# Kernel tuning notes

Hardware: AMD Instinct MI355X
Metric: run time of the kernel (lower is better)

The kernel has to match this reference:

```python
import jax, jax.numpy as jnp
import numpy as np

D, E, H, B, T, W = 64, 128, 64, 16, 512, 3
TEMP = 0.05


def setup_inputs() -> dict:
    key = jax.random.key(0)
    ks = jax.random.split(key, 11)
    s = 1.0 / np.sqrt(H)
    return {
        "x1": jax.random.normal(ks[0], (B, T, D), jnp.float32),
        "x2": jax.random.normal(ks[1], (B, T, D), jnp.float32),
        "u": jax.random.uniform(ks[2], (B, T), jnp.float32),
        "wih0": jax.random.normal(ks[3], (2, 4 * H, D), jnp.float32) * s,
        "whh0": jax.random.normal(ks[4], (2, 4 * H, H), jnp.float32) * s,
        "bih0": jax.random.normal(ks[5], (2, 4 * H), jnp.float32) * s,
        "bhh0": jax.random.normal(ks[6], (2, 4 * H), jnp.float32) * s,
        "wih1": jax.random.normal(ks[7], (2, 4 * H, 2 * H), jnp.float32) * s,
        "whh1": jax.random.normal(ks[8], (2, 4 * H, H), jnp.float32) * s,
        "bih1": jax.random.normal(ks[9], (2, 4 * H), jnp.float32) * s,
        "bhh1": jax.random.normal(ks[10], (2, 4 * H), jnp.float32) * s,
    }


def _lstm_dir(x, wi, wh, bi, bh, reverse):
    # x: [B, T, F]; PyTorch gate order i, f, g, o
    xg = jnp.einsum('btf,gf->btg', x, wi) + bi + bh  # [B, T, 4H]

    def step(carry, xg_t):
        h, c = carry
        g = xg_t + h @ wh.T
        i, f, gg, o = jnp.split(g, 4, axis=-1)
        c = jax.nn.sigmoid(f) * c + jax.nn.sigmoid(i) * jnp.tanh(gg)
        h = jax.nn.sigmoid(o) * jnp.tanh(c)
        return (h, c), h

    h0 = jnp.zeros((x.shape[0], H), x.dtype)
    _, hs = jax.lax.scan(step, (h0, h0), jnp.swapaxes(xg, 0, 1), reverse=reverse)
    return jnp.swapaxes(hs, 0, 1)  # [B, T, H]


def _bilstm_layer(x, wih, whh, bih, bhh):
    hf = _lstm_dir(x, wih[0], whh[0], bih[0], bhh[0], False)
    hb = _lstm_dir(x, wih[1], whh[1], bih[1], bhh[1], True)
    return jnp.concatenate([hf, hb], axis=-1)  # [B, T, 2H]


def _embed(x, wih0, whh0, bih0, bhh0, wih1, whh1, bih1, bhh1):
    h = _bilstm_layer(x, wih0, whh0, bih0, bhh0)
    h = _bilstm_layer(h, wih1, whh1, bih1, bhh1)
    # F.normalize(p=2, dim=-1), eps=1e-12
    n = jnp.maximum(jnp.linalg.norm(h, axis=-1, keepdims=True), 1e-12)
    return h / n


def _window_indices(u):
    # vectorized version of the per-step windowed np.random.choice
    # equal lengths: s = (len2 - len1 + 1) / (len1 - 1) = 1 / (T - 1)
    k = jnp.arange(T)
    s = 1.0 / (T - 1)
    center = k + (k * s).astype(jnp.int32)
    lo = jnp.maximum(center - W, 0)
    hi = jnp.minimum(center + W, T)       # slice end is clipped to list length
    count = (hi - lo).astype(jnp.float32)
    i2 = lo[None, :] + jnp.floor(u * count[None, :]).astype(jnp.int32)
    return jnp.minimum(i2, hi[None, :] - 1)  # [B, T]


def reference(x1, x2, u, wih0, whh0, bih0, bhh0, wih1, whh1, bih1, bhh1):
    z1 = _embed(x1, wih0, whh0, bih0, bhh0, wih1, whh1, bih1, bhh1)  # [B,T,E]
    z2 = _embed(x2, wih0, whh0, bih0, bhh0, wih1, whh1, bih1, bhh1)

    i2 = _window_indices(u)                                   # [B, T]
    z2s = jnp.take_along_axis(z2, i2[:, :, None], axis=1)     # [B, T, E]

    a = z1.reshape(-1, E)   # [N, E], N = B*T
    b = z2s.reshape(-1, E)

    # sim_matrix with eps-guarded renormalization (eps=1e-8)
    an = jnp.maximum(jnp.linalg.norm(a, axis=1, keepdims=True), 1e-8)
    bn = jnp.maximum(jnp.linalg.norm(b, axis=1, keepdims=True), 1e-8)
    sim = (a / an) @ (b / bn).T                               # [N, N]
    logits = sim / TEMP

    n = logits.shape[0]
    d = jnp.arange(n)
    lsm_row = jax.nn.log_softmax(logits, axis=1)
    lsm_col = jax.nn.log_softmax(logits, axis=0)
    loss = -(lsm_row[d, d].mean() + lsm_col[d, d].mean())
    return loss
```

## Files before the change

kernel.cpp:

```cpp
#include <hip/hip_runtime.h>
#include <hip/hip_bf16.h>

typedef unsigned short ushort_t;
typedef __attribute__((ext_vector_type(2))) float f32x2;
typedef __attribute__((ext_vector_type(4))) float f32x4;
typedef __attribute__((ext_vector_type(8))) short s16x8;
typedef _Float16 f16;
typedef __attribute__((ext_vector_type(2))) f16 f16x2;
typedef __attribute__((ext_vector_type(8))) f16 f16x8;

#define DEV __device__ __forceinline__

constexpr int MT = 16384;

DEV ushort_t f2bf(float f) {
  union { float f; unsigned u; } un; un.f = f;
  unsigned r = un.u + 0x7FFFu + ((un.u >> 16) & 1u);
  return (ushort_t)(r >> 16);
}
DEV ushort_t f2h(float f) {
  union { f16 h; ushort_t u; } cv; cv.h = (f16)f; return cv.u;
}
DEV float h2f(ushort_t u) {
  union { ushort_t u; f16 h; } cv; cv.u = u; return (float)cv.h;
}
template<int CTRL>
DEV float dppmv(float v) {
  union { float f; int i; } x; x.f = v;
  union { int i; float f; } y;
  y.i = __builtin_amdgcn_mov_dpp(x.i, CTRL, 0xf, 0xf, true);
  return y.f;
}
DEV int TPs(int rev, int t) {
  t = t > 511 ? 511 : t;
  t = t < 0 ? 0 : t;
  return rev ? (511 - t) : t;
}
DEV float sigf(float x) { return __builtin_amdgcn_rcpf(1.f + __expf(-x)); }
DEV float thf(float x)  { return 1.f - 2.f * __builtin_amdgcn_rcpf(1.f + __expf(2.f * x)); }
DEV float fexp2(float x) { float r; asm("v_exp_f32 %0, %1" : "=v"(r) : "v"(x)); return r; }

__global__ void k_idx(const float* __restrict__ u, int* __restrict__ i2) {
  int i = blockIdx.x * 256 + threadIdx.x;
  int t = i & 511;
  float s = 1.0f / 511.0f;
  int center = t + (int)((float)t * s);
  int lo = center - 3; if (lo < 0) lo = 0;
  int hi = center + 3; if (hi > 512) hi = 512;
  float count = (float)(hi - lo);
  int v = lo + (int)floorf(u[i] * count);
  int mx = hi - 1;
  i2[i] = v < mx ? v : mx;
}

__global__ void k_concat(const float* __restrict__ x1, const float* __restrict__ x2,
                         float* __restrict__ out) {
  int i = blockIdx.x * 256 + threadIdx.x;
  const int half = 16 * 512 * 64 / 4;
  float4* o = (float4*)out;
  const float4* a = (const float4*)x1;
  const float4* b = (const float4*)x2;
  o[i] = (i < half) ? a[i] : b[i - half];
}

template<int K>
__global__ __launch_bounds__(256) void k_xgemm(const float* __restrict__ In, const float* __restrict__ Wt,
                                               const float* __restrict__ bih, const float* __restrict__ bhh,
                                               ushort_t* __restrict__ Out) {
  const int bm = blockIdx.x, bn = blockIdx.y, d = blockIdx.z;
  const int tid = threadIdx.x;
  __shared__ float InS[64][128];
  __shared__ float WS[64][65];
  const int tm = tid >> 4, tn = tid & 15;
  float acc[8][4];
#pragma unroll
  for (int r = 0; r < 8; ++r)
#pragma unroll
    for (int c = 0; c < 4; ++c) acc[r][c] = 0.f;

  const int j = tid >> 2;
  const int jg = j >> 4, jt = j & 15;
  const int wn = jg * 64 + bn * 16 + jt;

  for (int kc = 0; kc < K; kc += 64) {
    __syncthreads();
    {
      const int m = tid >> 1;
      const float4* src = (const float4*)(In + (size_t)(bm * 128 + m) * K + kc);
#pragma unroll
      for (int i = 0; i < 8; ++i) {
        const int kq = (tid & 1) * 8 + i;
        float4 v = src[kq];
        InS[kq * 4 + 0][m] = v.x; InS[kq * 4 + 1][m] = v.y;
        InS[kq * 4 + 2][m] = v.z; InS[kq * 4 + 3][m] = v.w;
      }
      const float4* wsrc = (const float4*)(Wt + (size_t)(d * 256 + wn) * K + kc);
#pragma unroll
      for (int i = 0; i < 4; ++i) {
        const int kq = (tid & 3) * 4 + i;
        float4 v = wsrc[kq];
        WS[kq * 4 + 0][j] = v.x; WS[kq * 4 + 1][j] = v.y;
        WS[kq * 4 + 2][j] = v.z; WS[kq * 4 + 3][j] = v.w;
      }
    }
    __syncthreads();
#pragma unroll 8
    for (int k = 0; k < 64; ++k) {
      float4 a0 = *(const float4*)&InS[k][tm * 8];
      float4 a1 = *(const float4*)&InS[k][tm * 8 + 4];
      float av[8] = {a0.x, a0.y, a0.z, a0.w, a1.x, a1.y, a1.z, a1.w};
      float bb[4] = {WS[k][tn], WS[k][16 + tn], WS[k][32 + tn], WS[k][48 + tn]};
#pragma unroll
      for (int r = 0; r < 8; ++r)
#pragma unroll
        for (int c = 0; c < 4; ++c) acc[r][c] += av[r] * bb[c];
    }
  }
  const int u = bn * 16 + tn;
  float bs[4];
#pragma unroll
  for (int g = 0; g < 4; ++g)
    bs[g] = bih[d * 256 + g * 64 + u] + bhh[d * 256 + g * 64 + u];
  const int npb = bn * 64 + tn * 4;
#pragma unroll
  for (int r = 0; r < 8; ++r) {
    ushort4 o;
    o.x = f2h(acc[r][0] + bs[0]);
    o.y = f2h(acc[r][1] + bs[1]);
    o.z = f2h(acc[r][2] + bs[2]);
    o.w = f2h(acc[r][3] + bs[3]);
    *(ushort4*)(Out + ((size_t)d * MT + (size_t)(bm * 128 + tm * 8 + r)) * 256 + npb) = o;
  }
}

constexpr int NCH = 64;
constexpr int CH = 512 / NCH;
constexpr int WARM = 48;
__global__ __launch_bounds__(256) void k_scan10(const ushort_t* __restrict__ xg,
                                                const float* __restrict__ whh,
                                                float* __restrict__ hout) {
  __shared__ ushort_t H[2][1024] __attribute__((aligned(16)));
  const int tid = threadIdx.x;
  const int w = tid >> 6, l = tid & 63;
  const int cl = l & 15, rg = l >> 4;
  const int uq = cl >> 2, g = cl & 3;
  const int d = blockIdx.x >> 1, hf = blockIdx.x & 1;
  const int rev = d;
  const int s_begin = blockIdx.y * CH;
  const int wm = (s_begin < WARM) ? s_begin : WARM;
  const int sstart = s_begin - wm;
  const int nsteps = CH + wm;

  f16x8 Bf[4][2];
#pragma unroll
  for (int nt = 0; nt < 4; ++nt)
#pragma unroll
    for (int kc = 0; kc < 2; ++kc) {
      const int urow = g * 64 + (w * 16 + nt * 4 + uq);
      const float* src = whh + ((size_t)(d * 256 + urow)) * 64 + kc * 32 + rg * 8;
      f16x8 v;
#pragma unroll
      for (int i = 0; i < 8; ++i) v[i] = (f16)src[i];
      Bf[nt][kc] = v;
    }

  ((uint4*)H)[tid] = (uint4){0u, 0u, 0u, 0u};
  float c[4] = {0.f, 0.f, 0.f, 0.f};

  const size_t bbase = ((size_t)(d * 32 + hf * 16)) * 512 * 256;
  float* hcur = hout + ((size_t)(hf * 16) * 512 + (size_t)TPs(rev, sstart)) * 128 + d * 64;
  const int hdir = rev ? -128 : 128;
  int cx[4][4], ho[4];
#pragma unroll
  for (int nt = 0; nt < 4; ++nt) {
#pragma unroll
    for (int j = 0; j < 4; ++j)
      cx[nt][j] = ((rg * 4 + j) * 512) * 256 + w * 64 + nt * 16 + cl;
    ho[nt] = ((rg * 4 + g) * 512) * 128 + w * 16 + nt * 4 + uq;
  }
  const int ab0 = (cl * 128 + rg * 16) ^ ((cl & 7) << 4);
  const int ab1 = (cl * 128 + 64 + rg * 16) ^ ((cl & 7) << 4);
  const int hwoff_m = rg * 4 + g;
  const bool gb0 = (g & 1) != 0, gb1 = (g & 2) != 0;

  float pf0[4][4], pf1[4][4], pf2[4][4], pf3[4][4];
  auto LOADST = [&](int sp, float (&P)[4][4]) {
    const ushort_t* xp = xg + bbase + (size_t)TPs(rev, sstart + sp) * 256;
#pragma unroll
    for (int nt = 0; nt < 4; ++nt)
#pragma unroll
      for (int j = 0; j < 4; ++j) P[nt][j] = h2f(xp[cx[nt][j]]);
  };
  LOADST(0, pf0);
  LOADST(1, pf1);
  LOADST(2, pf2);

  asm volatile("s_waitcnt lgkmcnt(0)" ::: "memory");
  __builtin_amdgcn_s_barrier();
  asm volatile("" ::: "memory");

  auto STEP = [&](int s, float (&PC)[4][4], float (&PN)[4][4]) {
    const char* Hr = (const char*)H[s & 1];
    f16x8 a0 = *(const f16x8*)(Hr + ab0);
    f16x8 a1 = *(const f16x8*)(Hr + ab1);
    f32x4 acc[4];
#pragma unroll
    for (int nt = 0; nt < 4; ++nt) {
      acc[nt] = (f32x4){PC[nt][0], PC[nt][1], PC[nt][2], PC[nt][3]};
      acc[nt] = __builtin_amdgcn_mfma_f32_16x16x32_f16(a0, Bf[nt][0], acc[nt], 0, 0, 0);
      acc[nt] = __builtin_amdgcn_mfma_f32_16x16x32_f16(a1, Bf[nt][1], acc[nt], 0, 0, 0);
    }
    LOADST(s + 3, PN);
    char* Hw = (char*)H[(s & 1) ^ 1];
    float hv[4];
#pragma unroll
    for (int nt = 0; nt < 4; ++nt) {
      float V0 = acc[nt][0], V1 = acc[nt][1], V2 = acc[nt][2], V3 = acc[nt][3];
      float s0 = dppmv<0xB1>(V0);
      float s1 = dppmv<0xB1>(V1);
      float s2 = dppmv<0xB1>(V2);
      float s3 = dppmv<0xB1>(V3);
      asm volatile("" : "+v"(s0), "+v"(s1), "+v"(s2), "+v"(s3));
      float W0 = gb0 ? s1 : V0;
      float W1 = gb0 ? V1 : s0;
      float W2 = gb0 ? s3 : V2;
      float W3 = gb0 ? V3 : s2;
      float t0 = dppmv<0x4E>(W0);
      float t1 = dppmv<0x4E>(W1);
      float t2 = dppmv<0x4E>(W2);
      float t3 = dppmv<0x4E>(W3);
      asm volatile("" : "+v"(t0), "+v"(t1), "+v"(t2), "+v"(t3));
      float X0 = gb1 ? t2 : W0;
      float X1 = gb1 ? t3 : W1;
      float X2 = gb1 ? W2 : t0;
      float X3 = gb1 ? W3 : t1;
      const float si = sigf(X0), sf = sigf(X1), tg = thf(X2), so = sigf(X3);
      c[nt] = sf * c[nt] + si * tg;
      const float h = so * thf(c[nt]);
      hv[nt] = h;
      const int u = w * 16 + nt * 4 + uq;
      *(ushort_t*)(Hw + ((hwoff_m * 128 + u * 2) ^ ((hwoff_m & 7) << 4))) = f2h(h);
    }
    if (s >= wm) {
#pragma unroll
      for (int nt = 0; nt < 4; ++nt) hcur[ho[nt]] = hv[nt];
    }
    hcur += hdir;
    asm volatile("s_waitcnt lgkmcnt(0)" ::: "memory");
    __builtin_amdgcn_s_barrier();
    asm volatile("" ::: "memory");
  };

  for (int s = 0; s < nsteps; s += 4) {
    STEP(s + 0, pf0, pf3);
    STEP(s + 1, pf1, pf0);
    STEP(s + 2, pf2, pf1);
    STEP(s + 3, pf3, pf2);
  }
}

__global__ void k_norm(const float* __restrict__ h1, const int* __restrict__ i2,
                       ushort_t* __restrict__ A, ushort_t* __restrict__ Bm) {
  int rw = blockIdx.x * 4 + (threadIdx.x >> 6);
  int l = threadIdx.x & 63;
  int which = rw >> 13;
  int r = rw & 8191;
  const float* src;
  if (which == 0) {
    src = h1 + (size_t)r * 128;
  } else {
    int idx = i2[r];
    int b = r >> 9;
    src = h1 + ((size_t)((16 + b) * 512) + idx) * 128;
  }
  float2 v = *(const float2*)(src + l * 2);
  float ss = v.x * v.x + v.y * v.y;
#pragma unroll
  for (int m = 1; m < 64; m <<= 1) ss += __shfl_xor(ss, m, 64);
  float n = sqrtf(ss);
  n = n < 1e-12f ? 1e-12f : n;
  float inv = __builtin_amdgcn_rcpf(n);
  if (which == 0) inv *= 28.853900817779268f;
  ushort_t o0 = f2bf(v.x * inv), o1 = f2bf(v.y * inv);
  ushort_t* dst = (which ? Bm : A) + (size_t)r * 128 + l * 2;
  dst[0] = o0; dst[1] = o1;
}

__global__ __launch_bounds__(512) void k_flash(const ushort_t* __restrict__ A, const ushort_t* __restrict__ Bm,
                                               float* __restrict__ rowpart, float* __restrict__ colpart,
                                               float* __restrict__ diagl) {
  const int bid = blockIdx.x;
  const int swz = (bid & 7) * 512 + (bid >> 3);
  const int iblk = swz >> 6, jblk = swz & 63;
  __shared__ ushort_t As[128 * 128];
  __shared__ ushort_t Bs[128 * 128];
  __shared__ float rowbuf[4][128];
  __shared__ float colbuf[2][128];
  const int tid = threadIdx.x;
  {
    const int rr = tid >> 4, cq = tid & 15;
#pragma unroll
    for (int p = 0; p < 4; ++p) {
      const int row = p * 32 + rr;
      float4 va = *(const float4*)(A + ((size_t)(iblk * 128 + row)) * 128 + cq * 8);
      float4 vb = *(const float4*)(Bm + ((size_t)(jblk * 128 + row)) * 128 + cq * 8);
      const int byo = row * 256 + ((cq * 16) ^ ((row & 7) << 4));
      *(float4*)((char*)As + byo) = va;
      *(float4*)((char*)Bs + byo) = vb;
    }
  }
  __syncthreads();
  const int lane = tid & 63, wv = tid >> 6;
  const int wr = wv >> 2, wc = wv & 3;
  const int cl = lane & 15, q = lane >> 4;
  f32x4 acc[4][2];
#pragma unroll
  for (int mi = 0; mi < 4; ++mi)
#pragma unroll
    for (int ni = 0; ni < 2; ++ni) acc[mi][ni] = (f32x4){0.f, 0.f, 0.f, 0.f};

#pragma unroll
  for (int ks = 0; ks < 4; ++ks) {
    s16x8 af[4], bf[2];
#pragma unroll
    for (int mi = 0; mi < 4; ++mi) {
      const int row = wr * 64 + mi * 16 + cl;
      const int kb = ks * 64 + q * 16;
      af[mi] = *(const s16x8*)((const char*)As + row * 256 + (kb ^ ((row & 7) << 4)));
    }
#pragma unroll
    for (int ni = 0; ni < 2; ++ni) {
      const int row = wc * 32 + ni * 16 + cl;
      const int kb = ks * 64 + q * 16;
      bf[ni] = *(const s16x8*)((const char*)Bs + row * 256 + (kb ^ ((row & 7) << 4)));
    }
#pragma unroll
    for (int mi = 0; mi < 4; ++mi)
#pragma unroll
      for (int ni = 0; ni < 2; ++ni)
        acc[mi][ni] = __builtin_amdgcn_mfma_f32_16x16x32_bf16(af[mi], bf[ni], acc[mi][ni], 0, 0, 0);
  }
  float rowacc[4][4];
  float colacc[2] = {0.f, 0.f};
#pragma unroll
  for (int mi = 0; mi < 4; ++mi)
#pragma unroll
    for (int j = 0; j < 4; ++j) rowacc[mi][j] = 0.f;
#pragma unroll
  for (int mi = 0; mi < 4; ++mi)
#pragma unroll
    for (int ni = 0; ni < 2; ++ni)
#pragma unroll
      for (int j = 0; j < 4; ++j) {
        float e = fexp2(acc[mi][ni][j]);
        rowacc[mi][j] += e;
        colacc[ni] += e;
      }
  if (iblk == jblk) {
#pragma unroll
    for (int mi = 0; mi < 4; ++mi)
#pragma unroll
      for (int ni = 0; ni < 2; ++ni)
#pragma unroll
        for (int j = 0; j < 4; ++j)
          if ((wr * 64 + mi * 16 + q * 4 + j) == (wc * 32 + ni * 16 + cl))
            diagl[iblk * 128 + wr * 64 + mi * 16 + q * 4 + j] =
                acc[mi][ni][j] * 0.6931471805599453f;
  }
#pragma unroll
  for (int ni = 0; ni < 2; ++ni) {
    float r = colacc[ni];
    r += __shfl_xor(r, 16, 64);
    r += __shfl_xor(r, 32, 64);
    if (lane < 16) colbuf[wr][wc * 32 + ni * 16 + cl] = r;
  }
#pragma unroll
  for (int mi = 0; mi < 4; ++mi)
#pragma unroll
    for (int j = 0; j < 4; ++j) {
      float r = rowacc[mi][j];
      r += dppmv<0xB1>(r);
      r += dppmv<0x4E>(r);
      r += dppmv<0x141>(r);
      r += dppmv<0x140>(r);
      if (cl == 0) rowbuf[wc][wr * 64 + mi * 16 + q * 4 + j] = r;
    }
  __syncthreads();
  if (tid < 128) {
    rowpart[(size_t)jblk * 8192 + iblk * 128 + tid] =
        rowbuf[0][tid] + rowbuf[1][tid] + rowbuf[2][tid] + rowbuf[3][tid];
  } else if (tid < 256) {
    const int c2 = tid - 128;
    colpart[(size_t)iblk * 8192 + jblk * 128 + c2] = colbuf[0][c2] + colbuf[1][c2];
  }
}

__global__ void k_reduce(const float* __restrict__ rowpart, const float* __restrict__ colpart,
                         const float* __restrict__ diagl, float* __restrict__ bpart) {
  const int i = blockIdx.x * 256 + threadIdx.x;
  float sr = 0.f, sc = 0.f;
#pragma unroll 8
  for (int jb = 0; jb < 64; ++jb) {
    sr += rowpart[(size_t)jb * 8192 + i];
    sc += colpart[(size_t)jb * 8192 + i];
  }
  float term = 2.f * diagl[i] - __logf(sr) - __logf(sc);
#pragma unroll
  for (int m = 1; m < 64; m <<= 1) term += __shfl_xor(term, m, 64);
  __shared__ float red[4];
  if ((threadIdx.x & 63) == 0) red[threadIdx.x >> 6] = term;
  __syncthreads();
  if (threadIdx.x == 0) bpart[blockIdx.x] = red[0] + red[1] + red[2] + red[3];
}

__global__ void k_final(const float* __restrict__ bpart, float* __restrict__ out) {
  float v = (threadIdx.x < 32) ? bpart[threadIdx.x] : 0.f;
#pragma unroll
  for (int m = 1; m < 32; m <<= 1) v += __shfl_xor(v, m, 64);
  if (threadIdx.x == 0) out[0] = -v * (1.f / 8192.f);
}

extern "C" void kernel_launch(void* const* d_in, const int* in_sizes, int n_in,
                              void* d_out, int out_size, void* d_ws, size_t ws_size,
                              hipStream_t stream) {
  const float* x1   = (const float*)d_in[0];
  const float* x2   = (const float*)d_in[1];
  const float* u    = (const float*)d_in[2];
  const float* wih0 = (const float*)d_in[3];
  const float* whh0 = (const float*)d_in[4];
  const float* bih0 = (const float*)d_in[5];
  const float* bhh0 = (const float*)d_in[6];
  const float* wih1 = (const float*)d_in[7];
  const float* whh1 = (const float*)d_in[8];
  const float* bih1 = (const float*)d_in[9];
  const float* bhh1 = (const float*)d_in[10];
  float* out = (float*)d_out;

  char* ws = (char*)d_ws;
  ushort_t* xg = (ushort_t*)(ws);
  float* h0  = (float*)(ws + 33554432);
  float* in0 = (float*)(ws + 33554432 + 8388608);
  int*   i2  = (int*)(ws + 33554432 + 8388608 + 4194304);
  float* h1  = h0;
  ushort_t* Abf    = (ushort_t*)(ws);
  ushort_t* Bbf    = (ushort_t*)(ws + 2097152);
  float*    rowpart= (float*)(ws + 4194304);
  float*    colpart= (float*)(ws + 6291456);
  float*    diagl  = (float*)(ws + 8388608);
  float*    bpart  = (float*)(ws + 8421376);

  k_idx<<<32, 256, 0, stream>>>(u, i2);
  k_concat<<<1024, 256, 0, stream>>>(x1, x2, in0);
  k_xgemm<64><<<dim3(128, 4, 2), 256, 0, stream>>>(in0, wih0, bih0, bhh0, xg);
  k_scan10<<<dim3(4, NCH), 256, 0, stream>>>(xg, whh0, h0);
  k_xgemm<128><<<dim3(128, 4, 2), 256, 0, stream>>>(h0, wih1, bih1, bhh1, xg);
  k_scan10<<<dim3(4, NCH), 256, 0, stream>>>(xg, whh1, h1);
  k_norm<<<4096, 256, 0, stream>>>(h1, i2, Abf, Bbf);
  k_flash<<<4096, 512, 0, stream>>>(Abf, Bbf, rowpart, colpart, diagl);
  k_reduce<<<32, 256, 0, stream>>>(rowpart, colpart, diagl, bpart);
  k_final<<<1, 64, 0, stream>>>(bpart, out);
}
```

Measured before the change: 211.0 us.

## Swap MFMA operands so each lane holds all four gates; double scan chunks

Puts the recurrent weights in the A operand and the hidden state in B, so each lane's accumulator holds the i,f,g,o gates of one unit. This removes the per-step DPP cross-lane transposes and selects, and lets the gate-input loads become one ushort4 vector load per tile instead of four scalar loads. Separately, NCH rises from 64 to 128, which halves the chunk length and launches more blocks. Because the 48-step warm-up is fixed, this also adds proportionally more redundant warm-up steps per chunk.

```diff
diff --git a/kernel.cpp b/kernel.cpp
--- a/kernel.cpp
+++ b/kernel.cpp
@@ -133,7 +133,7 @@
   }
 }
 
-constexpr int NCH = 64;
+constexpr int NCH = 128;
 constexpr int CH = 512 / NCH;
 constexpr int WARM = 48;
 __global__ __launch_bounds__(256) void k_scan10(const ushort_t* __restrict__ xg,
@@ -143,7 +143,6 @@
   const int tid = threadIdx.x;
   const int w = tid >> 6, l = tid & 63;
   const int cl = l & 15, rg = l >> 4;
-  const int uq = cl >> 2, g = cl & 3;
   const int d = blockIdx.x >> 1, hf = blockIdx.x & 1;
   const int rev = d;
   const int s_begin = blockIdx.y * CH;
@@ -151,17 +150,17 @@
   const int sstart = s_begin - wm;
   const int nsteps = CH + wm;
 
-  f16x8 Bf[4][2];
+  f16x8 Af[4][2];
 #pragma unroll
   for (int nt = 0; nt < 4; ++nt)
 #pragma unroll
     for (int kc = 0; kc < 2; ++kc) {
-      const int urow = g * 64 + (w * 16 + nt * 4 + uq);
-      const float* src = whh + ((size_t)(d * 256 + urow)) * 64 + kc * 32 + rg * 8;
+      const int row_old = (cl & 3) * 64 + (w * 16 + nt * 4 + (cl >> 2));
+      const float* src = whh + ((size_t)(d * 256 + row_old)) * 64 + kc * 32 + rg * 8;
       f16x8 v;
 #pragma unroll
       for (int i = 0; i < 8; ++i) v[i] = (f16)src[i];
-      Bf[nt][kc] = v;
+      Af[nt][kc] = v;
     }
 
   ((uint4*)H)[tid] = (uint4){0u, 0u, 0u, 0u};
@@ -170,26 +169,26 @@
   const size_t bbase = ((size_t)(d * 32 + hf * 16)) * 512 * 256;
   float* hcur = hout + ((size_t)(hf * 16) * 512 + (size_t)TPs(rev, sstart)) * 128 + d * 64;
   const int hdir = rev ? -128 : 128;
-  int cx[4][4], ho[4];
+  int cx[4], ho[4], hw[4];
 #pragma unroll
   for (int nt = 0; nt < 4; ++nt) {
-#pragma unroll
-    for (int j = 0; j < 4; ++j)
-      cx[nt][j] = ((rg * 4 + j) * 512) * 256 + w * 64 + nt * 16 + cl;
-    ho[nt] = ((rg * 4 + g) * 512) * 128 + w * 16 + nt * 4 + uq;
+    cx[nt] = cl * (512 * 256) + w * 64 + nt * 16 + rg * 4;
+    const int unit = w * 16 + nt * 4 + rg;
+    ho[nt] = (cl * 512) * 128 + unit;
+    hw[nt] = (cl * 128 + unit * 2) ^ ((cl & 7) << 4);
   }
   const int ab0 = (cl * 128 + rg * 16) ^ ((cl & 7) << 4);
   const int ab1 = (cl * 128 + 64 + rg * 16) ^ ((cl & 7) << 4);
-  const int hwoff_m = rg * 4 + g;
-  const bool gb0 = (g & 1) != 0, gb1 = (g & 2) != 0;
 
   float pf0[4][4], pf1[4][4], pf2[4][4], pf3[4][4];
   auto LOADST = [&](int sp, float (&P)[4][4]) {
     const ushort_t* xp = xg + bbase + (size_t)TPs(rev, sstart + sp) * 256;
 #pragma unroll
-    for (int nt = 0; nt < 4; ++nt)
-#pragma unroll
-      for (int j = 0; j < 4; ++j) P[nt][j] = h2f(xp[cx[nt][j]]);
+    for (int nt = 0; nt < 4; ++nt) {
+      ushort4 v = *(const ushort4*)(xp + cx[nt]);
+      P[nt][0] = h2f(v.x); P[nt][1] = h2f(v.y);
+      P[nt][2] = h2f(v.z); P[nt][3] = h2f(v.w);
+    }
   };
   LOADST(0, pf0);
   LOADST(1, pf1);
@@ -201,45 +200,28 @@
 
   auto STEP = [&](int s, float (&PC)[4][4], float (&PN)[4][4]) {
     const char* Hr = (const char*)H[s & 1];
-    f16x8 a0 = *(const f16x8*)(Hr + ab0);
-    f16x8 a1 = *(const f16x8*)(Hr + ab1);
+    f16x8 b0 = *(const f16x8*)(Hr + ab0);
+    f16x8 b1 = *(const f16x8*)(Hr + ab1);
     f32x4 acc[4];
 #pragma unroll
     for (int nt = 0; nt < 4; ++nt) {
       acc[nt] = (f32x4){PC[nt][0], PC[nt][1], PC[nt][2], PC[nt][3]};
-      acc[nt] = __builtin_amdgcn_mfma_f32_16x16x32_f16(a0, Bf[nt][0], acc[nt], 0, 0, 0);
-      acc[nt] = __builtin_amdgcn_mfma_f32_16x16x32_f16(a1, Bf[nt][1], acc[nt], 0, 0, 0);
+      acc[nt] = __builtin_amdgcn_mfma_f32_16x16x32_f16(Af[nt][0], b0, acc[nt], 0, 0, 0);
+      acc[nt] = __builtin_amdgcn_mfma_f32_16x16x32_f16(Af[nt][1], b1, acc[nt], 0, 0, 0);
     }
     LOADST(s + 3, PN);
     char* Hw = (char*)H[(s & 1) ^ 1];
     float hv[4];
 #pragma unroll
     for (int nt = 0; nt < 4; ++nt) {
-      float V0 = acc[nt][0], V1 = acc[nt][1], V2 = acc[nt][2], V3 = acc[nt][3];
-      float s0 = dppmv<0xB1>(V0);
-      float s1 = dppmv<0xB1>(V1);
-      float s2 = dppmv<0xB1>(V2);
-      float s3 = dppmv<0xB1>(V3);
-      asm volatile("" : "+v"(s0), "+v"(s1), "+v"(s2), "+v"(s3));
-      float W0 = gb0 ? s1 : V0;
-      float W1 = gb0 ? V1 : s0;
-      float W2 = gb0 ? s3 : V2;
-      float W3 = gb0 ? V3 : s2;
-      float t0 = dppmv<0x4E>(W0);
-      float t1 = dppmv<0x4E>(W1);
-      float t2 = dppmv<0x4E>(W2);
-      float t3 = dppmv<0x4E>(W3);
-      asm volatile("" : "+v"(t0), "+v"(t1), "+v"(t2), "+v"(t3));
-      float X0 = gb1 ? t2 : W0;
-      float X1 = gb1 ? t3 : W1;
-      float X2 = gb1 ? W2 : t0;
-      float X3 = gb1 ? W3 : t1;
-      const float si = sigf(X0), sf = sigf(X1), tg = thf(X2), so = sigf(X3);
+      const float si = sigf(acc[nt][0]);
+      const float sf = sigf(acc[nt][1]);
+      const float tg = thf(acc[nt][2]);
+      const float so = sigf(acc[nt][3]);
       c[nt] = sf * c[nt] + si * tg;
       const float h = so * thf(c[nt]);
       hv[nt] = h;
-      const int u = w * 16 + nt * 4 + uq;
-      *(ushort_t*)(Hw + ((hwoff_m * 128 + u * 2) ^ ((hwoff_m & 7) << 4))) = f2h(h);
+      *(ushort_t*)(Hw + hw[nt]) = f2h(h);
     }
     if (s >= wm) {
 #pragma unroll
```

Result: slower. 231.7 us (+9.8%).
